# Performance work log

Measured on AMD Instinct MI355X. Metric: run time of the kernel, lower is better.

Reference implementation:

```python
import jax, jax.numpy as jnp
import numpy as np

EPSILON = 1e-36


def setup_inputs() -> dict:
    key = jax.random.key(0)
    k1, k2, k3, k4 = jax.random.split(key, 4)
    n, in_dim, out_dim = 8192, 128, 128
    x = jax.random.normal(k1, (n, in_dim), dtype=jnp.float32)
    # xavier-uniform-like scale for W_real
    limit = float(np.sqrt(6.0 / (in_dim + out_dim)))
    W_real = jax.random.uniform(k2, (in_dim, out_dim), dtype=jnp.float32, minval=-limit, maxval=limit)
    W_imag = jax.random.uniform(k3, (in_dim, out_dim), dtype=jnp.float32, minval=-0.1, maxval=0.1)
    G = jax.random.uniform(k4, (in_dim, out_dim), dtype=jnp.float32, minval=0.0, maxval=1.0)
    return {"x": x, "W_real": W_real, "W_imag": W_imag, "G": G}


def reference(x, W_real, W_imag, G):
    Gc = jnp.clip(G, 0.0, 1.0)                                   # (i,o)
    # R: (n,i,o) = |x| gated toward 1 by (1-G)
    R = (jnp.abs(x) + EPSILON)[:, :, None] * Gc[None] + (1.0 - Gc)[None]
    # K: pi where x<0, gated by G
    K = jnp.pi * (x < 0).astype(x.dtype)[:, :, None] * Gc[None]  # (n,i,o)
    logR = jnp.log(R)
    A = jnp.einsum('nio,io->no', logR, W_real) - jnp.einsum('nio,io->no', K, W_imag)
    B = jnp.einsum('nio,io->no', logR, W_imag) + jnp.einsum('nio,io->no', K, W_real)
    return jnp.exp(A) * jnp.cos(B)
```

## Files before the change

### kernel.cpp

```cpp
#include <hip/hip_runtime.h>
#include <math.h>


#define NROWS 8192
#define DIM   128
#define RPB   8
#define NT    512
#define IQ    32
#define PI_F  3.14159265358979323846f
#define LN2_F 0.69314718055994530942f

typedef float v2f __attribute__((ext_vector_type(2)));

static __device__ __forceinline__ v2f vfma2(v2f a, v2f b, v2f c) {
    return __builtin_elementwise_fma(a, b, c);
}

__global__ __launch_bounds__(256) void prep_w(
    const float* __restrict__ Wr, const float* __restrict__ Wi,
    const float* __restrict__ G, float4* __restrict__ wq,
    float* __restrict__ garr)
{
    int t = blockIdx.x * 256 + threadIdx.x;
    if (t < DIM * DIM) {
        float g  = fminf(fmaxf(G[t], 0.0f), 1.0f);
        float wr = Wr[t], wi = Wi[t];
        wq[t]   = make_float4(LN2_F * wr, LN2_F * wi, -g * wi, g * wr);
        garr[t] = g;
    }
}

template <bool PACKED>
__global__ __launch_bounds__(NT, 6) void main_kernel(
    const float* __restrict__ x, const float4* __restrict__ wq,
    const float* __restrict__ garr,
    const float* __restrict__ Wr, const float* __restrict__ Wi,
    const float* __restrict__ G, float* __restrict__ out)
{
    __shared__ float sbuf[2 * 4 * RPB * DIM];
    float* am1p = sbuf;
    float* psp  = sbuf + DIM * RPB;

    const int tid   = threadIdx.x;
    const int o     = tid & (DIM - 1);
    const int q     = tid >> 7;
    const int nbase = blockIdx.x * RPB;
    const float* xb = x + (size_t)nbase * DIM;

#pragma unroll
    for (int k = 0; k < 2; ++k) {
        int e = tid + k * NT;
        float xv = xb[e];
        int i = e & (DIM - 1), r = e >> 7;
        am1p[i * RPB + r] = fabsf(xv) - 1.0f;
        psp[i * RPB + r]  = (xv < 0.0f) ? PI_F : 0.0f;
    }
    __syncthreads();

    v2f accA[4], accB[4];
#pragma unroll
    for (int p = 0; p < 4; ++p) { accA[p] = (v2f){0.f, 0.f}; accB[p] = (v2f){0.f, 0.f}; }

    const int ibase = q * IQ;
#pragma unroll 2
    for (int ii = 0; ii < IQ; ++ii) {
        const int i = ibase + ii;
        float wrl, wil, ngwi, gwr, g;
        if (PACKED) {
            float4 w = wq[i * DIM + o];
            g = garr[i * DIM + o];
            wrl = w.x; wil = w.y; ngwi = w.z; gwr = w.w;
        } else {
            float wr = Wr[i * DIM + o], wi = Wi[i * DIM + o];
            g = fminf(fmaxf(G[i * DIM + o], 0.0f), 1.0f);
            wrl = LN2_F * wr; wil = LN2_F * wi; ngwi = -g * wi; gwr = g * wr;
        }
        const v2f gg2   = {g, g};
        const v2f wrl2  = {wrl, wrl};
        const v2f wil2  = {wil, wil};
        const v2f ngwi2 = {ngwi, ngwi};
        const v2f gwr2  = {gwr, gwr};
        const v2f one2  = {1.0f, 1.0f};

        const float4* a4 = (const float4*)(am1p + i * RPB);
        const float4* p4 = (const float4*)(psp  + i * RPB);
        float4 a03 = a4[0], a47 = a4[1];
        float4 s03 = p4[0], s47 = p4[1];

#define ROWPAIR(mx, my, sx, sy, idx)                                        \
        do {                                                                \
            v2f t2 = vfma2((v2f){mx, my}, gg2, one2);                       \
            v2f l2 = { __log2f(t2.x), __log2f(t2.y) };                      \
            v2f s2 = {sx, sy};                                              \
            accA[idx] = vfma2(l2, wrl2, vfma2(s2, ngwi2, accA[idx]));       \
            accB[idx] = vfma2(l2, wil2, vfma2(s2, gwr2,  accB[idx]));       \
        } while (0)

        ROWPAIR(a03.x, a03.y, s03.x, s03.y, 0);
        ROWPAIR(a03.z, a03.w, s03.z, s03.w, 1);
        ROWPAIR(a47.x, a47.y, s47.x, s47.y, 2);
        ROWPAIR(a47.z, a47.w, s47.z, s47.w, 3);
#undef ROWPAIR
    }

    __syncthreads();
    float* pA = sbuf;
    float* pB = sbuf + 4 * RPB * DIM;
#pragma unroll
    for (int p = 0; p < 4; ++p) {
        pA[q * (RPB * DIM) + (2 * p) * DIM + o]     = accA[p].x;
        pA[q * (RPB * DIM) + (2 * p + 1) * DIM + o] = accA[p].y;
        pB[q * (RPB * DIM) + (2 * p) * DIM + o]     = accB[p].x;
        pB[q * (RPB * DIM) + (2 * p + 1) * DIM + o] = accB[p].y;
    }
    __syncthreads();

    const int e  = tid * 2;
    const int r  = e >> 7, oo = e & (DIM - 1);
    v2f A = {0.f, 0.f}, B = {0.f, 0.f};
#pragma unroll
    for (int qq = 0; qq < 4; ++qq) {
        A += *(const v2f*)&pA[qq * (RPB * DIM) + r * DIM + oo];
        B += *(const v2f*)&pB[qq * (RPB * DIM) + r * DIM + oo];
    }
    float2 res;
    res.x = __expf(A.x) * __cosf(B.x);
    res.y = __expf(A.y) * __cosf(B.y);
    *(float2*)&out[(size_t)(nbase + r) * DIM + oo] = res;
}

extern "C" void kernel_launch(void* const* d_in, const int* in_sizes, int n_in,
                              void* d_out, int out_size, void* d_ws, size_t ws_size,
                              hipStream_t stream) {
    const float* x  = (const float*)d_in[0];
    const float* Wr = (const float*)d_in[1];
    const float* Wi = (const float*)d_in[2];
    const float* G  = (const float*)d_in[3];
    float* out = (float*)d_out;

    const size_t wq_bytes = (size_t)DIM * DIM * sizeof(float4);
    const size_t g_bytes  = (size_t)DIM * DIM * sizeof(float);
    if (ws_size >= wq_bytes + g_bytes) {
        float4* wq   = (float4*)d_ws;
        float*  garr = (float*)((char*)d_ws + wq_bytes);
        prep_w<<<(DIM * DIM + 255) / 256, 256, 0, stream>>>(Wr, Wi, G, wq, garr);
        main_kernel<true><<<NROWS / RPB, NT, 0, stream>>>(x, wq, garr,
                                                          nullptr, nullptr, nullptr, out);
    } else {
        main_kernel<false><<<NROWS / RPB, NT, 0, stream>>>(x, nullptr, nullptr,
                                                           Wr, Wi, G, out);
    }
}
```

Baseline: 86.61 us.

## Read x directly from global and drop LDS staging and a barrier

Removes the shared-memory staging of |x|-1 and sign values and the barrier that followed it. Each thread now reads its x values straight from global memory, which are uniform across the wave and likely become scalar loads. The gate term is packed as (g, 1-g) so the log argument is computed with a single fma, and the accumulators become scalar floats instead of packed pairs. Launch bounds rise to 8 waves per SIMD and the inner loop unroll goes from 2 to 4. The risks are more global load traffic per thread and losing packed-fma throughput.

```diff
diff --git a/kernel.cpp b/kernel.cpp
--- a/kernel.cpp
+++ b/kernel.cpp
@@ -12,111 +12,79 @@
 
 typedef float v2f __attribute__((ext_vector_type(2)));
 
-static __device__ __forceinline__ v2f vfma2(v2f a, v2f b, v2f c) {
-    return __builtin_elementwise_fma(a, b, c);
-}
-
 __global__ __launch_bounds__(256) void prep_w(
     const float* __restrict__ Wr, const float* __restrict__ Wi,
     const float* __restrict__ G, float4* __restrict__ wq,
-    float* __restrict__ garr)
+    float2* __restrict__ gq)
 {
     int t = blockIdx.x * 256 + threadIdx.x;
     if (t < DIM * DIM) {
         float g  = fminf(fmaxf(G[t], 0.0f), 1.0f);
         float wr = Wr[t], wi = Wi[t];
-        wq[t]   = make_float4(LN2_F * wr, LN2_F * wi, -g * wi, g * wr);
-        garr[t] = g;
+        wq[t] = make_float4(LN2_F * wr, LN2_F * wi, -g * wi, g * wr);
+        gq[t] = make_float2(g, 1.0f - g);
     }
 }
 
 template <bool PACKED>
-__global__ __launch_bounds__(NT, 6) void main_kernel(
+__global__ __launch_bounds__(NT, 8) void main_kernel(
     const float* __restrict__ x, const float4* __restrict__ wq,
-    const float* __restrict__ garr,
+    const float2* __restrict__ gq,
     const float* __restrict__ Wr, const float* __restrict__ Wi,
     const float* __restrict__ G, float* __restrict__ out)
 {
     __shared__ float sbuf[2 * 4 * RPB * DIM];
-    float* am1p = sbuf;
-    float* psp  = sbuf + DIM * RPB;
 
     const int tid   = threadIdx.x;
     const int o     = tid & (DIM - 1);
-    const int q     = tid >> 7;
+    const int q     = __builtin_amdgcn_readfirstlane(tid >> 7);
     const int nbase = blockIdx.x * RPB;
-    const float* xb = x + (size_t)nbase * DIM;
+    const int ibase = q * IQ;
 
+    const float* xb = x + (size_t)nbase * DIM + ibase;
+
+    float accA[RPB], accB[RPB];
 #pragma unroll
-    for (int k = 0; k < 2; ++k) {
-        int e = tid + k * NT;
-        float xv = xb[e];
-        int i = e & (DIM - 1), r = e >> 7;
-        am1p[i * RPB + r] = fabsf(xv) - 1.0f;
-        psp[i * RPB + r]  = (xv < 0.0f) ? PI_F : 0.0f;
+    for (int r = 0; r < RPB; ++r) { accA[r] = 0.0f; accB[r] = 0.0f; }
+
+#pragma unroll 4
+    for (int ii = 0; ii < IQ; ++ii) {
+        const int i = ibase + ii;
+        float wrl, wil, ngwi, gwr, g, onemg;
+        if (PACKED) {
+            float4 w  = wq[i * DIM + o];
+            float2 g2 = gq[i * DIM + o];
+            wrl = w.x; wil = w.y; ngwi = w.z; gwr = w.w;
+            g = g2.x; onemg = g2.y;
+        } else {
+            float wr = Wr[i * DIM + o], wi = Wi[i * DIM + o];
+            g = fminf(fmaxf(G[i * DIM + o], 0.0f), 1.0f);
+            onemg = 1.0f - g;
+            wrl = LN2_F * wr; wil = LN2_F * wi; ngwi = -g * wi; gwr = g * wr;
+        }
+#pragma unroll
+        for (int r = 0; r < RPB; ++r) {
+            float xv = xb[r * DIM + ii];
+            float ax = fabsf(xv);
+            float ps = (xv < 0.0f) ? PI_F : 0.0f;
+            float t  = fmaf(ax, g, onemg);
+            float l  = __log2f(t);
+            accA[r] = fmaf(l, wrl, fmaf(ps, ngwi, accA[r]));
+            accB[r] = fmaf(l, wil, fmaf(ps, gwr,  accB[r]));
+        }
+    }
+
+    float* pA = sbuf;
+    float* pB = sbuf + 4 * RPB * DIM;
+#pragma unroll
+    for (int r = 0; r < RPB; ++r) {
+        pA[q * (RPB * DIM) + r * DIM + o] = accA[r];
+        pB[q * (RPB * DIM) + r * DIM + o] = accB[r];
     }
     __syncthreads();
 
-    v2f accA[4], accB[4];
-#pragma unroll
-    for (int p = 0; p < 4; ++p) { accA[p] = (v2f){0.f, 0.f}; accB[p] = (v2f){0.f, 0.f}; }
-
-    const int ibase = q * IQ;
-#pragma unroll 2
-    for (int ii = 0; ii < IQ; ++ii) {
-        const int i = ibase + ii;
-        float wrl, wil, ngwi, gwr, g;
-        if (PACKED) {
-            float4 w = wq[i * DIM + o];
-            g = garr[i * DIM + o];
-            wrl = w.x; wil = w.y; ngwi = w.z; gwr = w.w;
-        } else {
-            float wr = Wr[i * DIM + o], wi = Wi[i * DIM + o];
-            g = fminf(fmaxf(G[i * DIM + o], 0.0f), 1.0f);
-            wrl = LN2_F * wr; wil = LN2_F * wi; ngwi = -g * wi; gwr = g * wr;
-        }
-        const v2f gg2   = {g, g};
-        const v2f wrl2  = {wrl, wrl};
-        const v2f wil2  = {wil, wil};
-        const v2f ngwi2 = {ngwi, ngwi};
-        const v2f gwr2  = {gwr, gwr};
-        const v2f one2  = {1.0f, 1.0f};
-
-        const float4* a4 = (const float4*)(am1p + i * RPB);
-        const float4* p4 = (const float4*)(psp  + i * RPB);
-        float4 a03 = a4[0], a47 = a4[1];
-        float4 s03 = p4[0], s47 = p4[1];
-
-#define ROWPAIR(mx, my, sx, sy, idx)                                        \
-        do {                                                                \
-            v2f t2 = vfma2((v2f){mx, my}, gg2, one2);                       \
-            v2f l2 = { __log2f(t2.x), __log2f(t2.y) };                      \
-            v2f s2 = {sx, sy};                                              \
-            accA[idx] = vfma2(l2, wrl2, vfma2(s2, ngwi2, accA[idx]));       \
-            accB[idx] = vfma2(l2, wil2, vfma2(s2, gwr2,  accB[idx]));       \
-        } while (0)
-
-        ROWPAIR(a03.x, a03.y, s03.x, s03.y, 0);
-        ROWPAIR(a03.z, a03.w, s03.z, s03.w, 1);
-        ROWPAIR(a47.x, a47.y, s47.x, s47.y, 2);
-        ROWPAIR(a47.z, a47.w, s47.z, s47.w, 3);
-#undef ROWPAIR
-    }
-
-    __syncthreads();
-    float* pA = sbuf;
-    float* pB = sbuf + 4 * RPB * DIM;
-#pragma unroll
-    for (int p = 0; p < 4; ++p) {
-        pA[q * (RPB * DIM) + (2 * p) * DIM + o]     = accA[p].x;
-        pA[q * (RPB * DIM) + (2 * p + 1) * DIM + o] = accA[p].y;
-        pB[q * (RPB * DIM) + (2 * p) * DIM + o]     = accB[p].x;
-        pB[q * (RPB * DIM) + (2 * p + 1) * DIM + o] = accB[p].y;
-    }
-    __syncthreads();
-
-    const int e  = tid * 2;
-    const int r  = e >> 7, oo = e & (DIM - 1);
+    const int c = tid * 2;
+    const int r = c >> 7, oo = c & (DIM - 1);
     v2f A = {0.f, 0.f}, B = {0.f, 0.f};
 #pragma unroll
     for (int qq = 0; qq < 4; ++qq) {
@@ -139,12 +107,12 @@
     float* out = (float*)d_out;
 
     const size_t wq_bytes = (size_t)DIM * DIM * sizeof(float4);
-    const size_t g_bytes  = (size_t)DIM * DIM * sizeof(float);
-    if (ws_size >= wq_bytes + g_bytes) {
-        float4* wq   = (float4*)d_ws;
-        float*  garr = (float*)((char*)d_ws + wq_bytes);
-        prep_w<<<(DIM * DIM + 255) / 256, 256, 0, stream>>>(Wr, Wi, G, wq, garr);
-        main_kernel<true><<<NROWS / RPB, NT, 0, stream>>>(x, wq, garr,
+    const size_t gq_bytes = (size_t)DIM * DIM * sizeof(float2);
+    if (ws_size >= wq_bytes + gq_bytes) {
+        float4* wq = (float4*)d_ws;
+        float2* gq = (float2*)((char*)d_ws + wq_bytes);
+        prep_w<<<(DIM * DIM + 255) / 256, 256, 0, stream>>>(Wr, Wi, G, wq, gq);
+        main_kernel<true><<<NROWS / RPB, NT, 0, stream>>>(x, wq, gq,
                                                           nullptr, nullptr, nullptr, out);
     } else {
         main_kernel<false><<<NROWS / RPB, NT, 0, stream>>>(x, nullptr, nullptr,
```

Result: slower. 92.68 us (+7.0%).

## Pack weights into one float4, halve LDS, and raise occupancy bound

Applied to the files above, without the earlier changes.

Packs the clipped gate into the float4 weight record so each iteration does one 16-byte load instead of a float4 plus a float, and recomputes the gated weights with two extra multiplies in the loop. The reduction now runs A and B through a single shared buffer in two phases, halving LDS per block, and launch bounds rise from 6 to 8 blocks per CU. The x load uses float2. This trades a little extra ALU and two more barriers for less memory traffic and higher occupancy, with a risk of register spilling under the tighter bound.

```diff
diff --git a/kernel.cpp b/kernel.cpp
--- a/kernel.cpp
+++ b/kernel.cpp
@@ -18,26 +18,22 @@
 
 __global__ __launch_bounds__(256) void prep_w(
     const float* __restrict__ Wr, const float* __restrict__ Wi,
-    const float* __restrict__ G, float4* __restrict__ wq,
-    float* __restrict__ garr)
+    const float* __restrict__ G, float4* __restrict__ wq)
 {
     int t = blockIdx.x * 256 + threadIdx.x;
     if (t < DIM * DIM) {
         float g  = fminf(fmaxf(G[t], 0.0f), 1.0f);
-        float wr = Wr[t], wi = Wi[t];
-        wq[t]   = make_float4(LN2_F * wr, LN2_F * wi, -g * wi, g * wr);
-        garr[t] = g;
+        wq[t] = make_float4(LN2_F * Wr[t], LN2_F * Wi[t], g, g * (1.0f / LN2_F));
     }
 }
 
 template <bool PACKED>
-__global__ __launch_bounds__(NT, 6) void main_kernel(
+__global__ __launch_bounds__(NT, 8) void main_kernel(
     const float* __restrict__ x, const float4* __restrict__ wq,
-    const float* __restrict__ garr,
     const float* __restrict__ Wr, const float* __restrict__ Wi,
     const float* __restrict__ G, float* __restrict__ out)
 {
-    __shared__ float sbuf[2 * 4 * RPB * DIM];
+    __shared__ float sbuf[4 * RPB * DIM];
     float* am1p = sbuf;
     float* psp  = sbuf + DIM * RPB;
 
@@ -47,13 +43,14 @@
     const int nbase = blockIdx.x * RPB;
     const float* xb = x + (size_t)nbase * DIM;
 
-#pragma unroll
-    for (int k = 0; k < 2; ++k) {
-        int e = tid + k * NT;
-        float xv = xb[e];
+    {
+        float2 v = ((const float2*)xb)[tid];
+        int e = tid * 2;
         int i = e & (DIM - 1), r = e >> 7;
-        am1p[i * RPB + r] = fabsf(xv) - 1.0f;
-        psp[i * RPB + r]  = (xv < 0.0f) ? PI_F : 0.0f;
+        am1p[i * RPB + r]       = fabsf(v.x) - 1.0f;
+        am1p[(i + 1) * RPB + r] = fabsf(v.y) - 1.0f;
+        psp[i * RPB + r]        = (v.x < 0.0f) ? PI_F : 0.0f;
+        psp[(i + 1) * RPB + r]  = (v.y < 0.0f) ? PI_F : 0.0f;
     }
     __syncthreads();
 
@@ -65,16 +62,18 @@
 #pragma unroll 2
     for (int ii = 0; ii < IQ; ++ii) {
         const int i = ibase + ii;
-        float wrl, wil, ngwi, gwr, g;
+        float wrl, wil, g, gq;
         if (PACKED) {
             float4 w = wq[i * DIM + o];
-            g = garr[i * DIM + o];
-            wrl = w.x; wil = w.y; ngwi = w.z; gwr = w.w;
+            wrl = w.x; wil = w.y; g = w.z; gq = w.w;
         } else {
-            float wr = Wr[i * DIM + o], wi = Wi[i * DIM + o];
-            g = fminf(fmaxf(G[i * DIM + o], 0.0f), 1.0f);
-            wrl = LN2_F * wr; wil = LN2_F * wi; ngwi = -g * wi; gwr = g * wr;
+            g   = fminf(fmaxf(G[i * DIM + o], 0.0f), 1.0f);
+            wrl = LN2_F * Wr[i * DIM + o];
+            wil = LN2_F * Wi[i * DIM + o];
+            gq  = g * (1.0f / LN2_F);
         }
+        const float ngwi = -gq * wil;
+        const float gwr  =  gq * wrl;
         const v2f gg2   = {g, g};
         const v2f wrl2  = {wrl, wrl};
         const v2f wil2  = {wil, wil};
@@ -103,26 +102,33 @@
 #undef ROWPAIR
     }
 
+    float* pP = sbuf;
+    const int c = tid * 2;
+    const int r = c >> 7, oo = c & (DIM - 1);
+
     __syncthreads();
-    float* pA = sbuf;
-    float* pB = sbuf + 4 * RPB * DIM;
 #pragma unroll
     for (int p = 0; p < 4; ++p) {
-        pA[q * (RPB * DIM) + (2 * p) * DIM + o]     = accA[p].x;
-        pA[q * (RPB * DIM) + (2 * p + 1) * DIM + o] = accA[p].y;
-        pB[q * (RPB * DIM) + (2 * p) * DIM + o]     = accB[p].x;
-        pB[q * (RPB * DIM) + (2 * p + 1) * DIM + o] = accB[p].y;
+        pP[q * (RPB * DIM) + (2 * p) * DIM + o]     = accA[p].x;
+        pP[q * (RPB * DIM) + (2 * p + 1) * DIM + o] = accA[p].y;
     }
     __syncthreads();
+    v2f A = {0.f, 0.f};
+#pragma unroll
+    for (int qq = 0; qq < 4; ++qq)
+        A += *(const v2f*)&pP[qq * (RPB * DIM) + r * DIM + oo];
+    __syncthreads();
+#pragma unroll
+    for (int p = 0; p < 4; ++p) {
+        pP[q * (RPB * DIM) + (2 * p) * DIM + o]     = accB[p].x;
+        pP[q * (RPB * DIM) + (2 * p + 1) * DIM + o] = accB[p].y;
+    }
+    __syncthreads();
+    v2f B = {0.f, 0.f};
+#pragma unroll
+    for (int qq = 0; qq < 4; ++qq)
+        B += *(const v2f*)&pP[qq * (RPB * DIM) + r * DIM + oo];
 
-    const int e  = tid * 2;
-    const int r  = e >> 7, oo = e & (DIM - 1);
-    v2f A = {0.f, 0.f}, B = {0.f, 0.f};
-#pragma unroll
-    for (int qq = 0; qq < 4; ++qq) {
-        A += *(const v2f*)&pA[qq * (RPB * DIM) + r * DIM + oo];
-        B += *(const v2f*)&pB[qq * (RPB * DIM) + r * DIM + oo];
-    }
     float2 res;
     res.x = __expf(A.x) * __cosf(B.x);
     res.y = __expf(A.y) * __cosf(B.y);
@@ -139,15 +145,13 @@
     float* out = (float*)d_out;
 
     const size_t wq_bytes = (size_t)DIM * DIM * sizeof(float4);
-    const size_t g_bytes  = (size_t)DIM * DIM * sizeof(float);
-    if (ws_size >= wq_bytes + g_bytes) {
-        float4* wq   = (float4*)d_ws;
-        float*  garr = (float*)((char*)d_ws + wq_bytes);
-        prep_w<<<(DIM * DIM + 255) / 256, 256, 0, stream>>>(Wr, Wi, G, wq, garr);
-        main_kernel<true><<<NROWS / RPB, NT, 0, stream>>>(x, wq, garr,
+    if (ws_size >= wq_bytes) {
+        float4* wq = (float4*)d_ws;
+        prep_w<<<(DIM * DIM + 255) / 256, 256, 0, stream>>>(Wr, Wi, G, wq);
+        main_kernel<true><<<NROWS / RPB, NT, 0, stream>>>(x, wq,
                                                           nullptr, nullptr, nullptr, out);
     } else {
-        main_kernel<false><<<NROWS / RPB, NT, 0, stream>>>(x, nullptr, nullptr,
+        main_kernel<false><<<NROWS / RPB, NT, 0, stream>>>(x, nullptr,
                                                            Wr, Wi, G, out);
     }
 }
```

Result: no change. 85.44 us (-1.4%).
